# Kernel tuning notes

Hardware: AMD Instinct MI355X
Metric: run time of the kernel (lower is better)

Reference implementation:

```python
import jax, jax.numpy as jnp
import numpy as np

DIM = 3
SIGMA_MIN = 0.05
NORM_EPS = 1e-10
DEG2RAD = np.pi / 180.0


def setup_inputs() -> dict:
    key = jax.random.key(0)
    kF, = jax.random.split(key, 1)
    B = 4_000_000
    F = jax.random.normal(kF, (B, 3, 3), dtype=jnp.float32)
    return {
        "F": F,
        "youngs_modulus_log": jnp.asarray(np.log(2_000_000.0), dtype=jnp.float32),
        "poissons_ratio": jnp.asarray(0.4, dtype=jnp.float32),
        "friction_angle": jnp.asarray(25.0, dtype=jnp.float32),
        "cohesion": jnp.asarray(0.0, dtype=jnp.float32),
    }


def reference(F, youngs_modulus_log, poissons_ratio, friction_angle, cohesion):
    E = jnp.exp(youngs_modulus_log)
    sin_phi = jnp.sin(friction_angle * DEG2RAD)
    alpha = jnp.sqrt(2.0 / 3.0) * 2.0 * sin_phi / (3.0 - sin_phi)
    mu = E / (2.0 * (1.0 + poissons_ratio))
    la = E * poissons_ratio / ((1.0 + poissons_ratio) * (1.0 - 2.0 * poissons_ratio))

    # Batched 3x3 SVD: U (B,3,3), sigma (B,3), Vh (B,3,3)
    U, sigma, Vh = jnp.linalg.svd(F, full_matrices=False)

    sigma = jnp.maximum(sigma, SIGMA_MIN)
    eps = jnp.log(sigma)                                   # log strain (B,3)
    trace = eps.sum(axis=1, keepdims=True)                 # (B,1)
    eps_hat = eps - trace / DIM                            # deviatoric part
    eps_hat_norm = jnp.maximum(
        jnp.linalg.norm(eps_hat, axis=1, keepdims=True), NORM_EPS)
    shifted_trace = trace - cohesion * DIM
    cond_yield = shifted_trace < 0.0                       # (B,1)
    delta_gamma = eps_hat_norm + (DIM * la + 2.0 * mu) / (2.0 * mu) * shifted_trace * alpha
    compress_eps = eps - jnp.maximum(delta_gamma, 0.0) / eps_hat_norm * eps_hat
    expand_eps = jnp.ones_like(eps) * cohesion
    eps_corrected = jnp.where(cond_yield, compress_eps, expand_eps)

    # F_corrected = U @ diag(exp(eps_corrected)) @ Vh
    F_corrected = jnp.einsum('bij,bj,bjk->bik', U, jnp.exp(eps_corrected), Vh)
    return F_corrected
```

## Files before the change

kernel.cpp:

```cpp
#include <hip/hip_runtime.h>
#include <math.h>

#define BLOCK 256
#define F4PB (BLOCK * 9 / 4)

__device__ __forceinline__ float frcp(float x)  { return __builtin_amdgcn_rcpf(x); }
__device__ __forceinline__ float frsq(float x)  { return __builtin_amdgcn_rsqf(x); }
__device__ __forceinline__ float fsqrt_r(float x){ return __builtin_amdgcn_sqrtf(x); }

__device__ __forceinline__ void rot(
    float& x0, float& x1, float& x2, float& np,
    float& y0, float& y1, float& y2, float& nq)
{
    float apq = fmaf(x0, y0, fmaf(x1, y1, x2 * y2));
    float del = np - nq;
    float rho = apq + apq;
    float r   = fsqrt_r(fmaf(del, del, rho * rho));
    float ch  = fabsf(del) + r + 1e-15f;
    bool  sw  = del < 0.0f;
    float sh  = sw ? -rho : rho;
    float inv = frsq(fmaf(ch, ch, sh * sh));
    float c   = ch * inv;
    float s   = sh * inv;
    float cf  = sw ? -s : c;
    float sf  = sw ?  c : s;
    float t;
    t = x0; x0 = fmaf(cf, t, sf * y0); y0 = fmaf(cf, y0, -sf * t);
    t = x1; x1 = fmaf(cf, t, sf * y1); y1 = fmaf(cf, y1, -sf * t);
    t = x2; x2 = fmaf(cf, t, sf * y2); y2 = fmaf(cf, y2, -sf * t);
    float sum = np + nq;
    np = 0.5f * (sum + r);
    nq = fmaxf(0.5f * (sum - r), 0.0f);
}

__global__ __launch_bounds__(BLOCK) void dp_kernel(
    const float* __restrict__ F,
    const float* __restrict__ p_yml,
    const float* __restrict__ p_nu,
    const float* __restrict__ p_fa,
    const float* __restrict__ p_coh,
    float* __restrict__ out,
    int n_elem)
{
    __shared__ float lds[BLOCK * 9];
    const int t_id    = threadIdx.x;
    const int nfloats = n_elem * 9;
    const int base_f  = (int)blockIdx.x * (BLOCK * 9);

    #pragma unroll
    for (int j = 0; j < 3; ++j) {
        int idx = t_id + j * BLOCK;
        if (idx < F4PB) {
            int g4 = (base_f >> 2) + idx;
            int gf = g4 << 2;
            if (gf + 4 <= nfloats) {
                ((float4*)lds)[idx] = ((const float4*)F)[g4];
            } else {
                #pragma unroll
                for (int k = 0; k < 4; ++k)
                    if (gf + k < nfloats) lds[idx * 4 + k] = F[gf + k];
            }
        }
    }
    __syncthreads();

    const int  e     = (int)blockIdx.x * BLOCK + t_id;
    const bool valid = e < n_elem;

    float a00, a01, a02, a10, a11, a12, a20, a21, a22;
    {
        const float* p = lds + t_id * 9;
        a00 = p[0]; a01 = p[1]; a02 = p[2];
        a10 = p[3]; a11 = p[4]; a12 = p[5];
        a20 = p[6]; a21 = p[7]; a22 = p[8];
    }

    const float yml = p_yml[0];
    const float nu  = p_nu[0];
    const float fa  = p_fa[0];
    const float coh = p_coh[0];
    const float E     = __expf(yml);
    const float sphi  = __sinf(fa * 0.017453292519943295f);
    const float alpha = 1.632993161855452f * sphi * frcp(3.0f - sphi);
    const float mu    = E * 0.5f * frcp(1.0f + nu);
    const float la    = E * nu * frcp((1.0f + nu) * (1.0f - 2.0f * nu));
    const float ratio = (3.0f * la + 2.0f * mu) * frcp(2.0f * mu) * alpha;

    float c00=a00, c10=a10, c20=a20;
    float c01=a01, c11=a11, c21=a21;
    float c02=a02, c12=a12, c22=a22;
    float n0 = fmaf(c00,c00, fmaf(c10,c10, c20*c20));
    float n1 = fmaf(c01,c01, fmaf(c11,c11, c21*c21));
    float n2 = fmaf(c02,c02, fmaf(c12,c12, c22*c22));

    #pragma unroll
    for (int sweep = 0; sweep < 4; ++sweep) {
        rot(c00,c10,c20,n0, c01,c11,c21,n1);
        rot(c00,c10,c20,n0, c02,c12,c22,n2);
        rot(c01,c11,c21,n1, c02,c12,c22,n2);
    }

    float i0 = frsq(fmaxf(n0, 1e-30f));
    float i1 = frsq(fmaxf(n1, 1e-30f));
    float u00 = c00*i0, u10 = c10*i0, u20 = c20*i0;
    float u01 = c01*i1, u11 = c11*i1, u21 = c21*i1;
    float u02 = fmaf(u10,u21, -u20*u11);
    float u12 = fmaf(u20,u01, -u00*u21);
    float u22 = fmaf(u00,u11, -u10*u01);

    float q0 = fmaf(a00,u00, fmaf(a10,u10, a20*u20));
    float q1 = fmaf(a01,u00, fmaf(a11,u10, a21*u20));
    float q2 = fmaf(a02,u00, fmaf(a12,u10, a22*u20));
    float m0 = fmaf(q0,q0, fmaf(q1,q1, q2*q2));
    float j0 = frsq(fmaxf(m0, 1e-30f));
    float v00 = q0*j0, v10 = q1*j0, v20 = q2*j0;

    q0 = fmaf(a00,u01, fmaf(a10,u11, a20*u21));
    q1 = fmaf(a01,u01, fmaf(a11,u11, a21*u21));
    q2 = fmaf(a02,u01, fmaf(a12,u11, a22*u21));
    float m1 = fmaf(q0,q0, fmaf(q1,q1, q2*q2));
    float j1 = frsq(fmaxf(m1, 1e-30f));
    float v01 = q0*j1, v11 = q1*j1, v21 = q2*j1;

    float v02 = fmaf(v10,v21, -v20*v11);
    float v12 = fmaf(v20,v01, -v00*v21);
    float v22 = fmaf(v00,v11, -v10*v01);

    float w0 = fmaf(a00,v02, fmaf(a01,v12, a02*v22));
    float w1 = fmaf(a10,v02, fmaf(a11,v12, a12*v22));
    float w2 = fmaf(a20,v02, fmaf(a21,v12, a22*v22));
    float s2 = fmaf(u02,w0, fmaf(u12,w1, u22*w2));

    float e0 = 0.5f * __logf(fmaxf(n0, 0.0025f));
    float e1 = 0.5f * __logf(fmaxf(n1, 0.0025f));
    float e2 = __logf(fmaxf(fabsf(s2), 0.05f));
    float tr  = e0 + e1 + e2;
    float tr3 = tr * (1.0f / 3.0f);
    float h0 = e0 - tr3, h1 = e1 - tr3, h2 = e2 - tr3;
    float hn = fsqrt_r(fmaf(h0,h0, fmaf(h1,h1, h2*h2)));
    hn = fmaxf(hn, 1e-10f);
    float st = tr - coh * 3.0f;
    float dg = hn + ratio * st;
    float sc = fmaxf(dg, 0.0f) * frcp(hn);
    bool yield = st < 0.0f;
    float ec0 = yield ? fmaf(-sc, h0, e0) : coh;
    float ec1 = yield ? fmaf(-sc, h1, e1) : coh;
    float ec2 = yield ? fmaf(-sc, h2, e2) : coh;
    float f0 = __expf(ec0);
    float f1 = __expf(ec1);
    float f2 = copysignf(__expf(ec2), s2);

    float w00 = u00*f0, w01 = u01*f1, w02 = u02*f2;
    float w10 = u10*f0, w11 = u11*f1, w12 = u12*f2;
    float w20 = u20*f0, w21 = u21*f1, w22 = u22*f2;
    float r00 = fmaf(w00,v00, fmaf(w01,v01, w02*v02));
    float r01 = fmaf(w00,v10, fmaf(w01,v11, w02*v12));
    float r02 = fmaf(w00,v20, fmaf(w01,v21, w02*v22));
    float r10 = fmaf(w10,v00, fmaf(w11,v01, w12*v02));
    float r11 = fmaf(w10,v10, fmaf(w11,v11, w12*v12));
    float r12 = fmaf(w10,v20, fmaf(w11,v21, w12*v22));
    float r20 = fmaf(w20,v00, fmaf(w21,v01, w22*v02));
    float r21 = fmaf(w20,v10, fmaf(w21,v11, w22*v12));
    float r22 = fmaf(w20,v20, fmaf(w21,v21, w22*v22));

    __syncthreads();
    if (valid) {
        float* p = lds + t_id * 9;
        p[0]=r00; p[1]=r01; p[2]=r02;
        p[3]=r10; p[4]=r11; p[5]=r12;
        p[6]=r20; p[7]=r21; p[8]=r22;
    }
    __syncthreads();

    #pragma unroll
    for (int j = 0; j < 3; ++j) {
        int idx = t_id + j * BLOCK;
        if (idx < F4PB) {
            int g4 = (base_f >> 2) + idx;
            int gf = g4 << 2;
            if (gf + 4 <= nfloats) {
                ((float4*)out)[g4] = ((float4*)lds)[idx];
            } else {
                #pragma unroll
                for (int k = 0; k < 4; ++k)
                    if (gf + k < nfloats) out[gf + k] = lds[idx * 4 + k];
            }
        }
    }
}

extern "C" void kernel_launch(void* const* d_in, const int* in_sizes, int n_in,
                              void* d_out, int out_size, void* d_ws, size_t ws_size,
                              hipStream_t stream) {
    const float* F = (const float*)d_in[0];
    const int n_elem = in_sizes[0] / 9;
    const int grid = (n_elem + BLOCK - 1) / BLOCK;
    dp_kernel<<<grid, BLOCK, 0, stream>>>(
        F,
        (const float*)d_in[1], (const float*)d_in[2],
        (const float*)d_in[3], (const float*)d_in[4],
        (float*)d_out, n_elem);
}
```

Measured before the change: 255.9 us.

## Replace Jacobi SVD with closed-form eigen solve of F^T F

Replaces the four-sweep one-sided Jacobi SVD with an analytic eigen-decomposition of the symmetric Gram matrix F^T F using the trigonometric cubic solution and cross-product eigenvectors. U is then recovered by normalizing F·v, and singular values come from the column norms. This cuts per-element ALU work in what appears to be a compute-bound kernel. The trade-off is lower accuracy from squaring the condition number and from the polynomial acos approximation, plus degenerate-case handling.

```diff
diff --git a/kernel.cpp b/kernel.cpp
--- a/kernel.cpp
+++ b/kernel.cpp
@@ -4,33 +4,43 @@
 #define BLOCK 256
 #define F4PB (BLOCK * 9 / 4)
 
-__device__ __forceinline__ float frcp(float x)  { return __builtin_amdgcn_rcpf(x); }
-__device__ __forceinline__ float frsq(float x)  { return __builtin_amdgcn_rsqf(x); }
+__device__ __forceinline__ float frcp(float x)   { return __builtin_amdgcn_rcpf(x); }
+__device__ __forceinline__ float frsq(float x)   { return __builtin_amdgcn_rsqf(x); }
 __device__ __forceinline__ float fsqrt_r(float x){ return __builtin_amdgcn_sqrtf(x); }
 
-__device__ __forceinline__ void rot(
-    float& x0, float& x1, float& x2, float& np,
-    float& y0, float& y1, float& y2, float& nq)
+__device__ __forceinline__ float acos_fast(float x) {
+    float ax = fabsf(x);
+    float p = fmaf(ax, -0.0187293f, 0.0742610f);
+    p = fmaf(ax, p, -0.2121144f);
+    p = fmaf(ax, p, 1.5707288f);
+    float r = fsqrt_r(fmaxf(1.0f - ax, 0.0f)) * p;
+    return (x < 0.0f) ? (3.14159265358979f - r) : r;
+}
+
+__device__ __forceinline__ void best_cross(
+    float r0x, float r0y, float r0z,
+    float r1x, float r1y, float r1z,
+    float r2x, float r2y, float r2z,
+    float& bx, float& by, float& bz, float& bn)
 {
-    float apq = fmaf(x0, y0, fmaf(x1, y1, x2 * y2));
-    float del = np - nq;
-    float rho = apq + apq;
-    float r   = fsqrt_r(fmaf(del, del, rho * rho));
-    float ch  = fabsf(del) + r + 1e-15f;
-    bool  sw  = del < 0.0f;
-    float sh  = sw ? -rho : rho;
-    float inv = frsq(fmaf(ch, ch, sh * sh));
-    float c   = ch * inv;
-    float s   = sh * inv;
-    float cf  = sw ? -s : c;
-    float sf  = sw ?  c : s;
-    float t;
-    t = x0; x0 = fmaf(cf, t, sf * y0); y0 = fmaf(cf, y0, -sf * t);
-    t = x1; x1 = fmaf(cf, t, sf * y1); y1 = fmaf(cf, y1, -sf * t);
-    t = x2; x2 = fmaf(cf, t, sf * y2); y2 = fmaf(cf, y2, -sf * t);
-    float sum = np + nq;
-    np = 0.5f * (sum + r);
-    nq = fmaxf(0.5f * (sum - r), 0.0f);
+    float c0x = fmaf(r0y,r1z, -r0z*r1y);
+    float c0y = fmaf(r0z,r1x, -r0x*r1z);
+    float c0z = fmaf(r0x,r1y, -r0y*r1x);
+    float c1x = fmaf(r0y,r2z, -r0z*r2y);
+    float c1y = fmaf(r0z,r2x, -r0x*r2z);
+    float c1z = fmaf(r0x,r2y, -r0y*r2x);
+    float c2x = fmaf(r1y,r2z, -r1z*r2y);
+    float c2y = fmaf(r1z,r2x, -r1x*r2z);
+    float c2z = fmaf(r1x,r2y, -r1y*r2x);
+    float n0 = fmaf(c0x,c0x, fmaf(c0y,c0y, c0z*c0z));
+    float n1 = fmaf(c1x,c1x, fmaf(c1y,c1y, c1z*c1z));
+    float n2 = fmaf(c2x,c2x, fmaf(c2y,c2y, c2z*c2z));
+    bool b1 = n1 > n0;
+    float sx = b1 ? c1x : c0x, sy = b1 ? c1y : c0y, sz = b1 ? c1z : c0z;
+    float sn = b1 ? n1 : n0;
+    bool b2 = n2 > sn;
+    bx = b2 ? c2x : sx; by = b2 ? c2y : sy; bz = b2 ? c2z : sz;
+    bn = b2 ? n2 : sn;
 }
 
 __global__ __launch_bounds__(BLOCK) void dp_kernel(
@@ -64,9 +74,6 @@
     }
     __syncthreads();
 
-    const int  e     = (int)blockIdx.x * BLOCK + t_id;
-    const bool valid = e < n_elem;
-
     float a00, a01, a02, a10, a11, a12, a20, a21, a22;
     {
         const float* p = lds + t_id * 9;
@@ -86,53 +93,89 @@
     const float la    = E * nu * frcp((1.0f + nu) * (1.0f - 2.0f * nu));
     const float ratio = (3.0f * la + 2.0f * mu) * frcp(2.0f * mu) * alpha;
 
-    float c00=a00, c10=a10, c20=a20;
-    float c01=a01, c11=a11, c21=a21;
-    float c02=a02, c12=a12, c22=a22;
-    float n0 = fmaf(c00,c00, fmaf(c10,c10, c20*c20));
-    float n1 = fmaf(c01,c01, fmaf(c11,c11, c21*c21));
-    float n2 = fmaf(c02,c02, fmaf(c12,c12, c22*c22));
-
-    #pragma unroll
-    for (int sweep = 0; sweep < 4; ++sweep) {
-        rot(c00,c10,c20,n0, c01,c11,c21,n1);
-        rot(c00,c10,c20,n0, c02,c12,c22,n2);
-        rot(c01,c11,c21,n1, c02,c12,c22,n2);
-    }
-
-    float i0 = frsq(fmaxf(n0, 1e-30f));
-    float i1 = frsq(fmaxf(n1, 1e-30f));
-    float u00 = c00*i0, u10 = c10*i0, u20 = c20*i0;
-    float u01 = c01*i1, u11 = c11*i1, u21 = c21*i1;
+    float s00 = fmaf(a00,a00, fmaf(a10,a10, a20*a20));
+    float s11 = fmaf(a01,a01, fmaf(a11,a11, a21*a21));
+    float s22 = fmaf(a02,a02, fmaf(a12,a12, a22*a22));
+    float s01 = fmaf(a00,a01, fmaf(a10,a11, a20*a21));
+    float s02 = fmaf(a00,a02, fmaf(a10,a12, a20*a22));
+    float s12 = fmaf(a01,a02, fmaf(a11,a12, a21*a22));
+
+    float q   = (s00 + s11 + s22) * (1.0f/3.0f);
+    float b00 = s00 - q, b11 = s11 - q, b22 = s22 - q;
+    float offsq = fmaf(s01,s01, fmaf(s02,s02, s12*s12));
+    float p2  = fmaf(b00,b00, fmaf(b11,b11, fmaf(b22,b22, 2.0f*offsq)));
+    float pp  = fsqrt_r(p2 * (1.0f/6.0f));
+    float pinv = frcp(fmaxf(pp, 1e-10f));
+    float det = b00*fmaf(b11,b22, -s12*s12)
+              - s01*fmaf(s01,b22, -s12*s02)
+              + s02*fmaf(s01,s12, -b11*s02);
+    float rdet = 0.5f * det * pinv * pinv * pinv;
+    rdet = fminf(fmaxf(rdet, -1.0f), 1.0f);
+    float phi  = acos_fast(rdet) * (1.0f/3.0f);
+    float lam0 = fmaf(2.0f*pp, __cosf(phi), q);
+    float lam2 = fmaf(2.0f*pp, __cosf(phi + 2.0943951023931953f), q);
+
+    float bx, by, bz, bn;
+    best_cross(s00-lam0, s01, s02,
+               s01, s11-lam0, s12,
+               s02, s12, s22-lam0, bx, by, bz, bn);
+    bool ok0 = bn > 1e-24f;
+    float ir0 = frsq(fmaxf(bn, 1e-30f));
+    float v00 = ok0 ? bx*ir0 : 1.0f;
+    float v10 = ok0 ? by*ir0 : 0.0f;
+    float v20 = ok0 ? bz*ir0 : 0.0f;
+
+    best_cross(s00-lam2, s01, s02,
+               s01, s11-lam2, s12,
+               s02, s12, s22-lam2, bx, by, bz, bn);
+    float axv = fabsf(v00), ayv = fabsf(v10), azv = fabsf(v20);
+    bool xm = (axv <= ayv) && (axv <= azv);
+    bool ym = (!xm) && (ayv <= azv);
+    float ex = xm ? 1.0f : 0.0f;
+    float ey = ym ? 1.0f : 0.0f;
+    float ez = (xm || ym) ? 0.0f : 1.0f;
+    float fx = fmaf(v10,ez, -v20*ey);
+    float fy = fmaf(v20,ex, -v00*ez);
+    float fz = fmaf(v00,ey, -v10*ex);
+    bool ok2 = bn > 1e-24f;
+    float wx = ok2 ? bx : fx, wy = ok2 ? by : fy, wz = ok2 ? bz : fz;
+    float dp = fmaf(wx,v00, fmaf(wy,v10, wz*v20));
+    wx = fmaf(-dp, v00, wx); wy = fmaf(-dp, v10, wy); wz = fmaf(-dp, v20, wz);
+    float wn = fmaf(wx,wx, fmaf(wy,wy, wz*wz));
+    bool okw = wn > 1e-24f;
+    wx = okw ? wx : fx; wy = okw ? wy : fy; wz = okw ? wz : fz;
+    wn = okw ? wn : fmaf(fx,fx, fmaf(fy,fy, fz*fz));
+    float irw = frsq(fmaxf(wn, 1e-30f));
+    float v02 = wx*irw, v12 = wy*irw, v22 = wz*irw;
+    float v01 = fmaf(v12,v20, -v22*v10);
+    float v11 = fmaf(v22,v00, -v02*v20);
+    float v21 = fmaf(v02,v10, -v12*v00);
+
+    float q0 = fmaf(a00,v00, fmaf(a01,v10, a02*v20));
+    float q1 = fmaf(a10,v00, fmaf(a11,v10, a12*v20));
+    float q2 = fmaf(a20,v00, fmaf(a21,v10, a22*v20));
+    float m0 = fmaf(q0,q0, fmaf(q1,q1, q2*q2));
+    float i0 = frsq(fmaxf(m0, 1e-30f));
+    float u00 = q0*i0, u10 = q1*i0, u20 = q2*i0;
+
+    q0 = fmaf(a00,v01, fmaf(a01,v11, a02*v21));
+    q1 = fmaf(a10,v01, fmaf(a11,v11, a12*v21));
+    q2 = fmaf(a20,v01, fmaf(a21,v11, a22*v21));
+    float m1 = fmaf(q0,q0, fmaf(q1,q1, q2*q2));
+    float i1 = frsq(fmaxf(m1, 1e-30f));
+    float u01 = q0*i1, u11 = q1*i1, u21 = q2*i1;
+
     float u02 = fmaf(u10,u21, -u20*u11);
     float u12 = fmaf(u20,u01, -u00*u21);
     float u22 = fmaf(u00,u11, -u10*u01);
-
-    float q0 = fmaf(a00,u00, fmaf(a10,u10, a20*u20));
-    float q1 = fmaf(a01,u00, fmaf(a11,u10, a21*u20));
-    float q2 = fmaf(a02,u00, fmaf(a12,u10, a22*u20));
-    float m0 = fmaf(q0,q0, fmaf(q1,q1, q2*q2));
-    float j0 = frsq(fmaxf(m0, 1e-30f));
-    float v00 = q0*j0, v10 = q1*j0, v20 = q2*j0;
-
-    q0 = fmaf(a00,u01, fmaf(a10,u11, a20*u21));
-    q1 = fmaf(a01,u01, fmaf(a11,u11, a21*u21));
-    q2 = fmaf(a02,u01, fmaf(a12,u11, a22*u21));
-    float m1 = fmaf(q0,q0, fmaf(q1,q1, q2*q2));
-    float j1 = frsq(fmaxf(m1, 1e-30f));
-    float v01 = q0*j1, v11 = q1*j1, v21 = q2*j1;
-
-    float v02 = fmaf(v10,v21, -v20*v11);
-    float v12 = fmaf(v20,v01, -v00*v21);
-    float v22 = fmaf(v00,v11, -v10*v01);
 
     float w0 = fmaf(a00,v02, fmaf(a01,v12, a02*v22));
     float w1 = fmaf(a10,v02, fmaf(a11,v12, a12*v22));
     float w2 = fmaf(a20,v02, fmaf(a21,v12, a22*v22));
     float s2 = fmaf(u02,w0, fmaf(u12,w1, u22*w2));
 
-    float e0 = 0.5f * __logf(fmaxf(n0, 0.0025f));
-    float e1 = 0.5f * __logf(fmaxf(n1, 0.0025f));
+    float e0 = 0.5f * __logf(fmaxf(m0, 0.0025f));
+    float e1 = 0.5f * __logf(fmaxf(m1, 0.0025f));
     float e2 = __logf(fmaxf(fabsf(s2), 0.05f));
     float tr  = e0 + e1 + e2;
     float tr3 = tr * (1.0f / 3.0f);
@@ -164,7 +207,7 @@
     float r22 = fmaf(w20,v20, fmaf(w21,v21, w22*v22));
 
     __syncthreads();
-    if (valid) {
+    {
         float* p = lds + t_id * 9;
         p[0]=r00; p[1]=r01; p[2]=r02;
         p[3]=r10; p[4]=r11; p[5]=r12;
```

Measured after the change: 258.1 us. About the same (+0.9%).
